# Kernel optimization log

Hardware: AMD Instinct MI355X
Metric: run time of the kernel (lower is better)

The kernel has to match this reference:

```python
import jax, jax.numpy as jnp
import numpy as np

B = 256
D, H, W = 15, 64, 128    # depth, latitude, longitude of input grid
d, h, w = 5, 16, 32      # grid after AveragePooling3D(3,4,4)
L_DEPTH = (d + 2) * h * w      # 3584
L_LON   = d * h * (w + 2)      # 2720
L_LAT   = d * (h + 2) * w      # 2880


def _local1d(xp, wt, bias):
    # Unshared-weight LocallyConnected1D(filters=1, kernel=3) + relu.
    # xp: (B, L+2) padded sequence; wt: (L, 3); bias: (L,)
    L = wt.shape[0]
    y = (wt[:, 0] * xp[:, 0:L]
         + wt[:, 1] * xp[:, 1:L + 1]
         + wt[:, 2] * xp[:, 2:L + 2]
         + bias)
    return jax.nn.relu(y)


def setup_inputs() -> dict:
    key = jax.random.key(0)
    ks = jax.random.split(key, 7)
    s = 0.1
    return {
        "x": jax.random.normal(ks[0], (B, D, H, W, 1), jnp.float32),
        "w_depth": jax.random.normal(ks[1], (L_DEPTH, 3), jnp.float32) * s,
        "b_depth": jax.random.normal(ks[2], (L_DEPTH,), jnp.float32) * s,
        "w_lon": jax.random.normal(ks[3], (L_LON, 3), jnp.float32) * s,
        "b_lon": jax.random.normal(ks[4], (L_LON,), jnp.float32) * s,
        "w_lat": jax.random.normal(ks[5], (L_LAT, 3), jnp.float32) * s,
        "b_lat": jax.random.normal(ks[6], (L_LAT,), jnp.float32) * s,
    }


def reference(x, w_depth, b_depth, w_lon, b_lon, w_lat, b_lat):
    Bn = x.shape[0]
    # AveragePooling3D(3,4,4): dims divide evenly -> reshape + mean
    xs = x.reshape(Bn, d, 3, h, 4, w, 4, 1).mean(axis=(2, 4, 6))  # (B,d,h,w,1)

    # ---- depth axis: pad depth, permute (3,2,1,4), flatten, local conv ----
    t = jnp.pad(xs, ((0, 0), (1, 1), (0, 0), (0, 0), (0, 0)))     # (B,d+2,h,w,1)
    t = jnp.transpose(t, (0, 3, 2, 1, 4))                         # (B,w,h,d+2,1)
    t = t.reshape(Bn, L_DEPTH)
    t = jnp.pad(t, ((0, 0), (1, 1)))                              # ZeroPadding1D(1)
    t = _local1d(t, w_depth, b_depth)
    t = t.reshape(Bn, w, h, d + 2, 1)
    t = jnp.transpose(t, (0, 3, 2, 1, 4))                         # (B,d+2,h,w,1)
    t = t[:, 1:-1]                                                # crop depth -> (B,d,h,w,1)

    # ---- longitude axis: pad last spatial dim, identity permute ----
    u = jnp.pad(t, ((0, 0), (0, 0), (0, 0), (1, 1), (0, 0)))      # (B,d,h,w+2,1)
    u = u.reshape(Bn, L_LON)
    u = jnp.pad(u, ((0, 0), (1, 1)))
    u = _local1d(u, w_lon, b_lon)
    u = u.reshape(Bn, d, h, w + 2, 1)
    u = u[:, :, :, 1:-1]                                          # (B,d,h,w,1)

    # ---- latitude axis: pad lat, permute (1,3,2,4) ----
    v = jnp.pad(u, ((0, 0), (0, 0), (1, 1), (0, 0), (0, 0)))      # (B,d,h+2,w,1)
    v = jnp.transpose(v, (0, 1, 3, 2, 4))                         # (B,d,w,h+2,1)
    v = v.reshape(Bn, L_LAT)
    v = jnp.pad(v, ((0, 0), (1, 1)))
    v = _local1d(v, w_lat, b_lat)
    v = v.reshape(Bn, d, w, h + 2, 1)
    v = jnp.transpose(v, (0, 1, 3, 2, 4))                         # (B,d,h+2,w,1)
    v = v[:, :, 1:-1]                                             # (B,d,h,w,1)

    # UpSampling3D(3,4,4): nearest-neighbor repeat
    out = jnp.broadcast_to(
        v[:, :, None, :, None, :, None, :],
        (Bn, d, 3, h, 4, w, 4, 1)
    ).reshape(Bn, D, H, W, 1)
    return out
```

## Files before the change

kernel.cpp:

```cpp
#include <hip/hip_runtime.h>


#define NELEM (15 * 64 * 128)
#define NCELL 2560

__global__ __launch_bounds__(256) void k_down(const float* __restrict__ x,
                                              float* __restrict__ ds)
{
    const int b  = blockIdx.y;
    const int c  = blockIdx.x * 256 + threadIdx.x;
    const int iw = c & 31;
    const int ih = (c >> 5) & 15;
    const int id = c >> 9;

    const float* p = x + (size_t)b * NELEM + ((id * 3) * 64 + ih * 4) * 128 + iw * 4;
    float s = 0.f;
    #pragma unroll
    for (int dd = 0; dd < 3; ++dd) {
        #pragma unroll
        for (int hh = 0; hh < 4; ++hh) {
            const float4 v = *reinterpret_cast<const float4*>(p + (dd * 64 + hh) * 128);
            s += (v.x + v.y) + (v.z + v.w);
        }
    }
    ds[(size_t)b * NCELL + c] = s * (1.f / 48.f);
}

__global__ __launch_bounds__(512) void k_rest(const float* __restrict__ ds,
                                              const float* __restrict__ wd,
                                              const float* __restrict__ bd,
                                              const float* __restrict__ wl,
                                              const float* __restrict__ bl,
                                              const float* __restrict__ wv,
                                              const float* __restrict__ bv,
                                              float* __restrict__ out)
{
    const int b   = blockIdx.y;
    const int dep = blockIdx.x;
    const int tid = threadIdx.x;

    __shared__ float ds3[3 * 512];
    __shared__ float u_lds[512];

    for (int i = tid; i < 3 * 512; i += 512) {
        const int kp = i >> 9;
        const int r  = i & 511;
        const int id = dep - 1 + kp;
        ds3[i] = (id >= 0 && id <= 4) ? ds[(size_t)b * NCELL + id * 512 + r] : 0.f;
    }
    __syncthreads();

    {
        const int ih = tid >> 5;
        const int iw = tid & 31;
        const float* dsr = ds3 + ih * 32;

        auto t1local = [&](int iwq) -> float {
            const int l = (iwq * 16 + ih) * 7 + dep + 1;
            const float y = wd[l * 3 + 0] * dsr[iwq]
                          + wd[l * 3 + 1] * dsr[512 + iwq]
                          + wd[l * 3 + 2] * dsr[1024 + iwq]
                          + bd[l];
            return fmaxf(y, 0.f);
        };
        auto ulon = [&](int kwq) -> float {
            return (kwq >= 1 && kwq <= 32) ? t1local(kwq - 1) : 0.f;
        };

        const int kw = iw + 1;
        const int m  = (dep * 16 + ih) * 34 + kw;
        const float y = wl[m * 3 + 0] * ulon(kw - 1)
                      + wl[m * 3 + 1] * ulon(kw)
                      + wl[m * 3 + 2] * ulon(kw + 1)
                      + bl[m];
        u_lds[tid] = fmaxf(y, 0.f);
    }
    __syncthreads();

    {
        const int ihh = tid >> 5;
        const int iww = tid & 31;
        const int n   = (dep * 32 + iww) * 18 + ihh + 1;

        const float x0 = (ihh > 0)  ? u_lds[(ihh - 1) * 32 + iww] : 0.f;
        const float x1 =              u_lds[ihh * 32 + iww];
        const float x2 = (ihh < 15) ? u_lds[(ihh + 1) * 32 + iww] : 0.f;
        const float y  = fmaxf(wv[n * 3 + 0] * x0 + wv[n * 3 + 1] * x1
                             + wv[n * 3 + 2] * x2 + bv[n], 0.f);
        const float4 y4 = make_float4(y, y, y, y);

        float4* ob = reinterpret_cast<float4*>(out + (size_t)b * NELEM);
        #pragma unroll
        for (int dd = 0; dd < 3; ++dd) {
            #pragma unroll
            for (int hh = 0; hh < 4; ++hh) {
                ob[((dep * 3 + dd) * 64 + ihh * 4 + hh) * 32 + iww] = y4;
            }
        }
    }
}

extern "C" void kernel_launch(void* const* d_in, const int* in_sizes, int n_in,
                              void* d_out, int out_size, void* d_ws, size_t ws_size,
                              hipStream_t stream) {
    const float* x       = (const float*)d_in[0];
    const float* w_depth = (const float*)d_in[1];
    const float* b_depth = (const float*)d_in[2];
    const float* w_lon   = (const float*)d_in[3];
    const float* b_lon   = (const float*)d_in[4];
    const float* w_lat   = (const float*)d_in[5];
    const float* b_lat   = (const float*)d_in[6];
    float* out = (float*)d_out;

    const int Bn = in_sizes[0] / NELEM;

    float* ds = (float*)d_ws;

    k_down<<<dim3(NCELL / 256, Bn), dim3(256), 0, stream>>>(x, ds);
    k_rest<<<dim3(5, Bn), dim3(512), 0, stream>>>(ds, w_depth, b_depth,
                                                  w_lon, b_lon, w_lat, b_lat, out);
}
```

Measured before the change: 231.4 us.

## Split pooling per thread-row and upsample writes per depth plane with nontemporal stores

The pooling kernel now gives each of 384 threads one float4 load and reduces the 12 partial sums through shared memory, instead of having each thread issue 12 strided loads. The second kernel launches one block per output depth plane (15 instead of 5 per batch) with 256 threads. Each block recomputes the small stencil chain for its plane and writes its slice with nontemporal vector stores. This adds parallelism and memory-level concurrency at the cost of recomputing the stencil three times, an extra barrier, and a mostly idle reduction step.

```diff
diff --git a/kernel.cpp b/kernel.cpp
--- a/kernel.cpp
+++ b/kernel.cpp
@@ -4,45 +4,53 @@
 #define NELEM (15 * 64 * 128)
 #define NCELL 2560
 
-__global__ __launch_bounds__(256) void k_down(const float* __restrict__ x,
+typedef float vfloat4 __attribute__((ext_vector_type(4)));
+
+__global__ __launch_bounds__(384) void k_down(const float* __restrict__ x,
                                               float* __restrict__ ds)
 {
     const int b  = blockIdx.y;
-    const int c  = blockIdx.x * 256 + threadIdx.x;
-    const int iw = c & 31;
-    const int ih = (c >> 5) & 15;
-    const int id = c >> 9;
+    const int cr = blockIdx.x;
+    const int id = cr >> 4;
+    const int ih = cr & 15;
+    const int tid = threadIdx.x;
+    const int iw = tid & 31;
+    const int hh = (tid >> 5) & 3;
+    const int dd = tid >> 7;
 
-    const float* p = x + (size_t)b * NELEM + ((id * 3) * 64 + ih * 4) * 128 + iw * 4;
-    float s = 0.f;
-    #pragma unroll
-    for (int dd = 0; dd < 3; ++dd) {
+    __shared__ float part[12][32];
+
+    const vfloat4 v = *reinterpret_cast<const vfloat4*>(
+        x + (size_t)b * NELEM + ((size_t)((id * 3 + dd) * 64 + ih * 4 + hh)) * 128 + iw * 4);
+    part[dd * 4 + hh][iw] = (v.x + v.y) + (v.z + v.w);
+    __syncthreads();
+
+    if (tid < 32) {
+        float s = 0.f;
         #pragma unroll
-        for (int hh = 0; hh < 4; ++hh) {
-            const float4 v = *reinterpret_cast<const float4*>(p + (dd * 64 + hh) * 128);
-            s += (v.x + v.y) + (v.z + v.w);
-        }
+        for (int j = 0; j < 12; ++j) s += part[j][tid];
+        ds[(size_t)b * NCELL + (id * 16 + ih) * 32 + tid] = s * (1.f / 48.f);
     }
-    ds[(size_t)b * NCELL + c] = s * (1.f / 48.f);
 }
 
-__global__ __launch_bounds__(512) void k_rest(const float* __restrict__ ds,
-                                              const float* __restrict__ wd,
-                                              const float* __restrict__ bd,
-                                              const float* __restrict__ wl,
-                                              const float* __restrict__ bl,
-                                              const float* __restrict__ wv,
-                                              const float* __restrict__ bv,
-                                              float* __restrict__ out)
+__global__ __launch_bounds__(256) void k_plane(const float* __restrict__ ds,
+                                               const float* __restrict__ wd,
+                                               const float* __restrict__ bd,
+                                               const float* __restrict__ wl,
+                                               const float* __restrict__ bl,
+                                               const float* __restrict__ wv,
+                                               const float* __restrict__ bv,
+                                               float* __restrict__ out)
 {
-    const int b   = blockIdx.y;
-    const int dep = blockIdx.x;
-    const int tid = threadIdx.x;
+    const int b      = blockIdx.y;
+    const int dplane = blockIdx.x;
+    const int dep    = dplane / 3;
+    const int tid    = threadIdx.x;
 
     __shared__ float ds3[3 * 512];
     __shared__ float u_lds[512];
 
-    for (int i = tid; i < 3 * 512; i += 512) {
+    for (int i = tid; i < 3 * 512; i += 256) {
         const int kp = i >> 9;
         const int r  = i & 511;
         const int id = dep - 1 + kp;
@@ -50,9 +58,10 @@
     }
     __syncthreads();
 
-    {
-        const int ih = tid >> 5;
-        const int iw = tid & 31;
+    #pragma unroll
+    for (int c = tid; c < 512; c += 256) {
+        const int ih = c >> 5;
+        const int iw = c & 31;
         const float* dsr = ds3 + ih * 32;
 
         auto t1local = [&](int iwq) -> float {
@@ -73,13 +82,14 @@
                       + wl[m * 3 + 1] * ulon(kw)
                       + wl[m * 3 + 2] * ulon(kw + 1)
                       + bl[m];
-        u_lds[tid] = fmaxf(y, 0.f);
+        u_lds[c] = fmaxf(y, 0.f);
     }
     __syncthreads();
 
-    {
-        const int ihh = tid >> 5;
-        const int iww = tid & 31;
+    #pragma unroll
+    for (int c = tid; c < 512; c += 256) {
+        const int ihh = c >> 5;
+        const int iww = c & 31;
         const int n   = (dep * 32 + iww) * 18 + ihh + 1;
 
         const float x0 = (ihh > 0)  ? u_lds[(ihh - 1) * 32 + iww] : 0.f;
@@ -87,15 +97,14 @@
         const float x2 = (ihh < 15) ? u_lds[(ihh + 1) * 32 + iww] : 0.f;
         const float y  = fmaxf(wv[n * 3 + 0] * x0 + wv[n * 3 + 1] * x1
                              + wv[n * 3 + 2] * x2 + bv[n], 0.f);
-        const float4 y4 = make_float4(y, y, y, y);
+        vfloat4 y4;
+        y4.x = y; y4.y = y; y4.z = y; y4.w = y;
 
-        float4* ob = reinterpret_cast<float4*>(out + (size_t)b * NELEM);
+        float* pb = out + (size_t)b * NELEM
+                  + ((size_t)dplane * 64 + ihh * 4) * 128 + iww * 4;
         #pragma unroll
-        for (int dd = 0; dd < 3; ++dd) {
-            #pragma unroll
-            for (int hh = 0; hh < 4; ++hh) {
-                ob[((dep * 3 + dd) * 64 + ihh * 4 + hh) * 32 + iww] = y4;
-            }
+        for (int hhh = 0; hhh < 4; ++hhh) {
+            __builtin_nontemporal_store(y4, reinterpret_cast<vfloat4*>(pb + hhh * 128));
         }
     }
 }
@@ -116,7 +125,7 @@
 
     float* ds = (float*)d_ws;
 
-    k_down<<<dim3(NCELL / 256, Bn), dim3(256), 0, stream>>>(x, ds);
-    k_rest<<<dim3(5, Bn), dim3(512), 0, stream>>>(ds, w_depth, b_depth,
-                                                  w_lon, b_lon, w_lat, b_lat, out);
+    k_down <<<dim3(80, Bn), dim3(384), 0, stream>>>(x, ds);
+    k_plane<<<dim3(15, Bn), dim3(256), 0, stream>>>(ds, w_depth, b_depth,
+                                                    w_lon, b_lon, w_lat, b_lat, out);
 }
```

Measured after the change: 238.1 us. +2.9%, slower.

## Fuse average pooling into the per-depth kernel and drop the intermediate buffer

Applied to the files above, without the earlier changes.

Merges the pooling kernel into the local-conv/upsample kernel so each block pools its three needed depth slices directly from the input. This removes one kernel launch and the workspace write/read of the pooled grid. In exchange, neighboring depth slices are pooled redundantly by adjacent blocks, increasing input reads, and block size halves with each thread handling multiple cells.

```diff
diff --git a/kernel.cpp b/kernel.cpp
--- a/kernel.cpp
+++ b/kernel.cpp
@@ -4,36 +4,14 @@
 #define NELEM (15 * 64 * 128)
 #define NCELL 2560
 
-__global__ __launch_bounds__(256) void k_down(const float* __restrict__ x,
-                                              float* __restrict__ ds)
-{
-    const int b  = blockIdx.y;
-    const int c  = blockIdx.x * 256 + threadIdx.x;
-    const int iw = c & 31;
-    const int ih = (c >> 5) & 15;
-    const int id = c >> 9;
-
-    const float* p = x + (size_t)b * NELEM + ((id * 3) * 64 + ih * 4) * 128 + iw * 4;
-    float s = 0.f;
-    #pragma unroll
-    for (int dd = 0; dd < 3; ++dd) {
-        #pragma unroll
-        for (int hh = 0; hh < 4; ++hh) {
-            const float4 v = *reinterpret_cast<const float4*>(p + (dd * 64 + hh) * 128);
-            s += (v.x + v.y) + (v.z + v.w);
-        }
-    }
-    ds[(size_t)b * NCELL + c] = s * (1.f / 48.f);
-}
-
-__global__ __launch_bounds__(512) void k_rest(const float* __restrict__ ds,
-                                              const float* __restrict__ wd,
-                                              const float* __restrict__ bd,
-                                              const float* __restrict__ wl,
-                                              const float* __restrict__ bl,
-                                              const float* __restrict__ wv,
-                                              const float* __restrict__ bv,
-                                              float* __restrict__ out)
+__global__ __launch_bounds__(256) void k_all(const float* __restrict__ x,
+                                             const float* __restrict__ wd,
+                                             const float* __restrict__ bd,
+                                             const float* __restrict__ wl,
+                                             const float* __restrict__ bl,
+                                             const float* __restrict__ wv,
+                                             const float* __restrict__ bv,
+                                             float* __restrict__ out)
 {
     const int b   = blockIdx.y;
     const int dep = blockIdx.x;
@@ -42,17 +20,35 @@
     __shared__ float ds3[3 * 512];
     __shared__ float u_lds[512];
 
-    for (int i = tid; i < 3 * 512; i += 512) {
-        const int kp = i >> 9;
-        const int r  = i & 511;
+    const float* xb = x + (size_t)b * NELEM;
+    #pragma unroll
+    for (int c = tid; c < 3 * 512; c += 256) {
+        const int kp = c >> 9;
+        const int r  = c & 511;
+        const int ih = r >> 5;
+        const int iw = r & 31;
         const int id = dep - 1 + kp;
-        ds3[i] = (id >= 0 && id <= 4) ? ds[(size_t)b * NCELL + id * 512 + r] : 0.f;
+        float s = 0.f;
+        if (id >= 0 && id <= 4) {
+            const float* p = xb + ((size_t)(id * 3) * 64 + ih * 4) * 128 + iw * 4;
+            #pragma unroll
+            for (int dd = 0; dd < 3; ++dd) {
+                #pragma unroll
+                for (int hh = 0; hh < 4; ++hh) {
+                    const float4 v = *reinterpret_cast<const float4*>(p + (dd * 64 + hh) * 128);
+                    s += (v.x + v.y) + (v.z + v.w);
+                }
+            }
+            s *= (1.f / 48.f);
+        }
+        ds3[c] = s;
     }
     __syncthreads();
 
-    {
-        const int ih = tid >> 5;
-        const int iw = tid & 31;
+    #pragma unroll
+    for (int c = tid; c < 512; c += 256) {
+        const int ih = c >> 5;
+        const int iw = c & 31;
         const float* dsr = ds3 + ih * 32;
 
         auto t1local = [&](int iwq) -> float {
@@ -73,13 +69,15 @@
                       + wl[m * 3 + 1] * ulon(kw)
                       + wl[m * 3 + 2] * ulon(kw + 1)
                       + bl[m];
-        u_lds[tid] = fmaxf(y, 0.f);
+        u_lds[c] = fmaxf(y, 0.f);
     }
     __syncthreads();
 
-    {
-        const int ihh = tid >> 5;
-        const int iww = tid & 31;
+    float* ob = out + (size_t)b * NELEM;
+    #pragma unroll
+    for (int c = tid; c < 512; c += 256) {
+        const int ihh = c >> 5;
+        const int iww = c & 31;
         const int n   = (dep * 32 + iww) * 18 + ihh + 1;
 
         const float x0 = (ihh > 0)  ? u_lds[(ihh - 1) * 32 + iww] : 0.f;
@@ -89,12 +87,12 @@
                              + wv[n * 3 + 2] * x2 + bv[n], 0.f);
         const float4 y4 = make_float4(y, y, y, y);
 
-        float4* ob = reinterpret_cast<float4*>(out + (size_t)b * NELEM);
+        float* pb = ob + ((size_t)(dep * 3) * 64 + ihh * 4) * 128 + iww * 4;
         #pragma unroll
         for (int dd = 0; dd < 3; ++dd) {
             #pragma unroll
             for (int hh = 0; hh < 4; ++hh) {
-                ob[((dep * 3 + dd) * 64 + ihh * 4 + hh) * 32 + iww] = y4;
+                *reinterpret_cast<float4*>(pb + (dd * 64 + hh) * 128) = y4;
             }
         }
     }
@@ -114,9 +112,6 @@
 
     const int Bn = in_sizes[0] / NELEM;
 
-    float* ds = (float*)d_ws;
-
-    k_down<<<dim3(NCELL / 256, Bn), dim3(256), 0, stream>>>(x, ds);
-    k_rest<<<dim3(5, Bn), dim3(512), 0, stream>>>(ds, w_depth, b_depth,
-                                                  w_lon, b_lon, w_lat, b_lat, out);
+    k_all<<<dim3(5, Bn), dim3(256), 0, stream>>>(x, w_depth, b_depth,
+                                                 w_lon, b_lon, w_lat, b_lat, out);
 }
```

Result: slower. 242.4 us (+4.8%).
